# Performance work log

Measured on AMD Instinct MI355X. Metric: run time of the kernel, lower is better.

## Reference

```python
import jax, jax.numpy as jnp
import numpy as np

L, D_IN, D_OUT, H = 4096, 512, 256, 4
HEAD = D_OUT // H  # 64


def setup_inputs() -> dict:
    key = jax.random.key(0)
    k1, k2, k3, k4, k5 = jax.random.split(key, 5)
    h = jax.random.normal(k1, (L, D_IN), dtype=jnp.float32)
    A = jax.random.randint(k2, (L, L), 0, 2, dtype=jnp.int32)
    W = jax.random.normal(k3, (D_OUT, D_IN), dtype=jnp.float32) * 0.05
    attn = jax.random.normal(k4, (H, 2 * HEAD), dtype=jnp.float32) * 0.05
    out_w = jax.random.normal(k5, (D_OUT, D_OUT), dtype=jnp.float32) * 0.05
    out_b = jnp.zeros((D_OUT,), dtype=jnp.float32)
    return {"h": h, "A": A, "W": W, "attn": attn, "out_w": out_w, "out_b": out_b}


def reference(h, A, W, attn, out_w, out_b):
    # h: (L, D_in), A: (L, L) in {0,1}
    Lq = h.shape[0]
    n_heads, two_d = attn.shape
    d = two_d // 2
    Wh = (h @ W.T).reshape(Lq, n_heads, d)  # (L, H, d)
    # Algebraic rewrite of concat-score: e_ij = a1.Wh_i + a2.Wh_j
    a1, a2 = attn[:, :d], attn[:, d:]
    s_i = jnp.einsum("lhd,hd->lh", Wh, a1)  # (L, H)
    s_j = jnp.einsum("lhd,hd->lh", Wh, a2)  # (L, H)
    e = jax.nn.leaky_relu(s_i[:, None, :] + s_j[None, :, :], negative_slope=0.2)  # (L, L, H)
    mask = (A > 0)[:, :, None]  # (L, L, 1)
    NEG = jnp.asarray(-1e30, e.dtype)
    e = jnp.where(mask, e, NEG)
    # stable masked softmax over j (axis=1); rows with no neighbors -> alpha = 0
    m = jnp.max(e, axis=1, keepdims=True)
    m = jnp.where(m > NEG / 2, m, 0.0)
    ex = jnp.where(mask, jnp.exp(e - m), 0.0)
    denom = jnp.sum(ex, axis=1, keepdims=True)
    alpha = ex / jnp.where(denom > 0, denom, 1.0)  # (L, L, H)
    # dropout is identity in eval mode
    out = jnp.einsum("ijh,jhd->ihd", alpha, Wh).reshape(Lq, n_heads * d)
    return out @ out_w.T + out_b
```

## Files before the change

### kernel.cpp

```cpp
#include <hip/hip_runtime.h>
#include <hip/hip_bf16.h>

#define L_    4096
#define DIN   512
#define DOUT  256
#define NH    4
#define HD    64
#define JW    128

typedef unsigned short u16;
typedef __attribute__((ext_vector_type(8))) short short8;
typedef __attribute__((ext_vector_type(4))) float floatx4;

__device__ __forceinline__ float bf2f(u16 u) {
  union { unsigned u32; float f; } v; v.u32 = ((unsigned)u) << 16; return v.f;
}
__device__ __forceinline__ u16 f2bf(float f) {
  union { float f; unsigned u; } v; v.f = f;
  unsigned r = v.u + 0x7fff + ((v.u >> 16) & 1);
  return (u16)(r >> 16);
}
__device__ __forceinline__ unsigned cvt2(float a, float b) {
  __hip_bfloat162 v = __float22bfloat162_rn(make_float2(a, b));
  return *reinterpret_cast<unsigned*>(&v);
}
__device__ __forceinline__ short8 pack8(const float* __restrict__ p) {
  float4 a = *(const float4*)p, b = *(const float4*)(p + 4);
  union { unsigned u[4]; short8 s; } r;
  r.u[0] = cvt2(a.x, a.y); r.u[1] = cvt2(a.z, a.w);
  r.u[2] = cvt2(b.x, b.y); r.u[3] = cvt2(b.z, b.w);
  return r.s;
}

__device__ __forceinline__ void mfma_cdmap(int lane, int* rowm, int* colm) {
  const int c0 = lane & 15;
  union { u16 u[8]; short8 s; } a1, b1, a2, b2;
  const u16 one = f2bf(1.f), cid = f2bf((float)c0);
  #pragma unroll
  for (int j = 0; j < 8; ++j) { a1.u[j] = cid; b1.u[j] = one; a2.u[j] = one; b2.u[j] = cid; }
  floatx4 z = {0.f, 0.f, 0.f, 0.f};
  floatx4 dr = __builtin_amdgcn_mfma_f32_16x16x32_bf16(a1.s, b1.s, z, 0, 0, 0);
  floatx4 dc = __builtin_amdgcn_mfma_f32_16x16x32_bf16(a2.s, b2.s, z, 0, 0, 0);
  #pragma unroll
  for (int r = 0; r < 4; ++r) {
    rowm[r] = (int)(dr[r] * 0.03125f + 0.5f);
    colm[r] = (int)(dc[r] * 0.03125f + 0.5f);
  }
}

__global__ __launch_bounds__(256) void k0b_wf(const float* __restrict__ W,
                                              u16* __restrict__ Wf) {
  const int g = blockIdx.x * 256 + threadIdx.x;
  const int col = g >> 4, kblock = g & 15;
  const int cg = col >> 6, nt = (col >> 4) & 3, c0 = col & 15;
  const float* src = W + (size_t)col * DIN + kblock * 32;
  u16* dst = Wf + ((size_t)(cg * 4 + nt) * 16 + kblock) * 512 + c0 * 8;
  #pragma unroll
  for (int q = 0; q < 4; ++q) {
    short8 v = pack8(src + q * 8);
    *(short8*)(dst + q * 128) = v;
  }
}

__global__ __launch_bounds__(1024) void k1_wh(
    const float* __restrict__ h, const u16* __restrict__ Wf,
    const float* __restrict__ attn,
    u16* __restrict__ WhTf, float* __restrict__ s1g, float2* __restrict__ bdg)
{
  const int i0 = blockIdx.x * 16;
  const int t = threadIdx.x;
  const int wv = t >> 6, lane = t & 63, q = lane >> 4, c0 = lane & 15;
  const int cg = wv & 3, kc = wv >> 2;
  int rowm[4], colm[4];
  mfma_cdmap(lane, rowm, colm);

  __shared__ u16  hT[16][DIN + 8];
  __shared__ float pA[16][DOUT + 8];
  __shared__ float pB[16][DOUT + 8];
  __shared__ float attnL[NH * 128];

  if (t < 512) attnL[t] = attn[t];
  {
    const int row = t >> 6, c8 = (t & 63) * 8;
    const float* hp = h + (size_t)(i0 + row) * DIN + c8;
    float4 a = *(const float4*)hp;
    float4 b = *(const float4*)(hp + 4);
    union { unsigned u[4]; int4 v; } pk;
    pk.u[0] = cvt2(a.x, a.y); pk.u[1] = cvt2(a.z, a.w);
    pk.u[2] = cvt2(b.x, b.y); pk.u[3] = cvt2(b.z, b.w);
    *(int4*)&hT[row][c8] = pk.v;
  }
  __syncthreads();

  floatx4 acc[4] = {};
  #pragma unroll
  for (int ktl = 0; ktl < 4; ++ktl) {
    const int kb = kc * 128 + ktl * 32 + q * 8;
    short8 af = *(const short8*)&hT[c0][kb];
    #pragma unroll
    for (int nt = 0; nt < 4; ++nt) {
      short8 bf = *(const short8*)(Wf + ((size_t)(cg * 4 + nt) * 16 + kc * 4 + ktl) * 512 + lane * 8);
      acc[nt] = __builtin_amdgcn_mfma_f32_16x16x32_bf16(af, bf, acc[nt], 0, 0, 0);
    }
  }

  auto writeT = [&](float (*P)[DOUT + 8]) {
    #pragma unroll
    for (int nt = 0; nt < 4; ++nt)
      #pragma unroll
      for (int r = 0; r < 4; ++r)
        P[rowm[r]][cg * 64 + nt * 16 + colm[r]] = acc[nt][r];
  };
  auto addB2A = [&]() {
    const int row = t >> 6, c4 = (t & 63) * 4;
    float4* a = (float4*)&pA[row][c4];
    float4 bv = *(float4*)&pB[row][c4];
    float4 av = *a;
    av.x += bv.x; av.y += bv.y; av.z += bv.z; av.w += bv.w;
    *a = av;
  };

  if (kc == 0) writeT(pA);
  if (kc == 1) writeT(pB);
  __syncthreads();
  addB2A();
  __syncthreads();
  if (kc == 2) writeT(pB);
  __syncthreads();
  addB2A();
  __syncthreads();
  if (kc == 3) writeT(pB);
  __syncthreads();
  addB2A();
  __syncthreads();

  if (t < 64) {
    const int r = t & 15, hh = t >> 4;
    float s1 = 0.f, s2 = 0.f;
    for (int d = 0; d < HD; ++d) {
      float v = pA[r][hh * 64 + d];
      s1 += v * attnL[hh * 128 + d];
      s2 += v * attnL[hh * 128 + 64 + d];
    }
    s1g[hh * L_ + i0 + r] = s1;
    bdg[hh * L_ + i0 + r] = make_float2(__expf(s2), __expf(0.2f * s2));
  }

  if (t < 256) {
    const int d = t;
    const int hd = d >> 6, nt = (d >> 4) & 3, dc0 = d & 15;
    const int jblock = i0 >> 5, qbase = (i0 & 31) >> 3;
    u16* base = WhTf + ((size_t)(hd * 4 + nt) * JW + jblock) * 512 + dc0 * 8;
    #pragma unroll
    for (int jh = 0; jh < 2; ++jh) {
      const int i = jh * 8;
      union { unsigned u[4]; int4 v; } pk;
      pk.u[0] = cvt2(pA[i + 0][d], pA[i + 1][d]);
      pk.u[1] = cvt2(pA[i + 2][d], pA[i + 3][d]);
      pk.u[2] = cvt2(pA[i + 4][d], pA[i + 5][d]);
      pk.u[3] = cvt2(pA[i + 6][d], pA[i + 7][d]);
      *(int4*)(base + (qbase + jh) * 128) = pk.v;
    }
  }
}

__global__ __launch_bounds__(1024) void k2_attn(
    const int* __restrict__ A, const u16* __restrict__ WhTf,
    const float* __restrict__ s1g, const float2* __restrict__ bdg,
    const float* __restrict__ out_w, const float* __restrict__ out_b,
    float* __restrict__ out)
{
  const int i0 = blockIdx.x * 16;
  const int t = threadIdx.x;
  const int wv = t >> 6, lane = t & 63, q = lane >> 4, c0 = lane & 15;
  const int hd = wv & 3, jc = wv >> 2;
  int rowm[4], colm[4];
  mfma_cdmap(lane, rowm, colm);

  __shared__ float pA[NH][16][HD + 4];
  __shared__ float pB[NH][16][HD + 4];
  __shared__ float dden[NH][4][16];
  __shared__ float rcpS[NH][16];
  __shared__ u16  CnL[16][DOUT + 8];
  __shared__ unsigned AbitL[16][JW + 2];

  {
    const int row = t >> 6, ln = t & 63;
    const int* Ar = A + (size_t)(i0 + row) * L_;
    #pragma unroll
    for (int wsel = 0; wsel < 2; ++wsel) {
      const int wI = ln * 2 + wsel;
      const int* p = Ar + wI * 32;
      unsigned bits = 0u;
      #pragma unroll
      for (int wd = 0; wd < 8; ++wd) {
        int4 v = *(const int4*)(p + wd * 4);
        bits |= (v.x > 0 ? 1u : 0u) << (wd * 4 + 0);
        bits |= (v.y > 0 ? 1u : 0u) << (wd * 4 + 1);
        bits |= (v.z > 0 ? 1u : 0u) << (wd * 4 + 2);
        bits |= (v.w > 0 ? 1u : 0u) << (wd * 4 + 3);
      }
      AbitL[row][wI] = bits;
    }
  }
  __syncthreads();

  const float s1v = s1g[hd * L_ + i0 + c0];
  const float av = __expf(s1v);
  const float cv = __expf(0.2f * s1v);
  const float th = __expf(-s1v);
  const float2* bdh = bdg + (size_t)hd * L_;
  const u16* Wc = WhTf + (size_t)(hd * 4) * JW * 512 + (size_t)(jc * 32) * 512 + lane * 8;

  floatx4 acc[4] = {};
  float dpart = 0.f;
  const int jbase = jc * 1024;

  for (int kt = 0; kt < 32; ++kt) {
    const int kb = jbase + kt * 32 + q * 8;
    float4 v0 = *(const float4*)(bdh + kb);
    float4 v1 = *(const float4*)(bdh + kb + 2);
    float4 v2 = *(const float4*)(bdh + kb + 4);
    float4 v3 = *(const float4*)(bdh + kb + 6);
    const float bb[8] = {v0.x, v0.z, v1.x, v1.z, v2.x, v2.z, v3.x, v3.z};
    const float dd[8] = {v0.y, v0.w, v1.y, v1.w, v2.y, v2.w, v3.y, v3.w};
    const unsigned mbits = (AbitL[c0][jc * 32 + kt] >> (q * 8)) & 0xffu;
    float ex[8];
    #pragma unroll
    for (int jj = 0; jj < 8; ++jj) {
      float p = (bb[jj] >= th) ? (av * bb[jj]) : (cv * dd[jj]);
      ex[jj] = ((mbits >> jj) & 1u) ? p : 0.f;
      dpart += ex[jj];
    }
    union { unsigned u[4]; short8 s; } pf;
    pf.u[0] = cvt2(ex[0], ex[1]); pf.u[1] = cvt2(ex[2], ex[3]);
    pf.u[2] = cvt2(ex[4], ex[5]); pf.u[3] = cvt2(ex[6], ex[7]);
    #pragma unroll
    for (int nt = 0; nt < 4; ++nt) {
      short8 bfr = *(const short8*)(Wc + ((size_t)nt * JW + kt) * 512);
      acc[nt] = __builtin_amdgcn_mfma_f32_16x16x32_bf16(pf.s, bfr, acc[nt], 0, 0, 0);
    }
  }

  dpart += __shfl_xor(dpart, 16, 64);
  dpart += __shfl_xor(dpart, 32, 64);
  if (lane < 16) dden[hd][jc][lane] = dpart;

  auto writeT = [&](float (*P)[HD + 4]) {
    #pragma unroll
    for (int nt = 0; nt < 4; ++nt)
      #pragma unroll
      for (int r = 0; r < 4; ++r)
        P[rowm[r]][nt * 16 + colm[r]] = acc[nt][r];
  };
  auto addB2A = [&]() {
    const int h2 = t >> 8, rem = t & 255, row = rem >> 4, d4 = (rem & 15) * 4;
    float4* a = (float4*)&pA[h2][row][d4];
    float4 bv = *(float4*)&pB[h2][row][d4];
    float4 av2 = *a;
    av2.x += bv.x; av2.y += bv.y; av2.z += bv.z; av2.w += bv.w;
    *a = av2;
  };

  if (jc == 0) writeT(pA[hd]);
  if (jc == 1) writeT(pB[hd]);
  __syncthreads();
  if (t < 64) {
    const int hh = t >> 4, r = t & 15;
    float den = dden[hh][0][r] + dden[hh][1][r] + dden[hh][2][r] + dden[hh][3][r];
    rcpS[hh][r] = (den > 0.f) ? (1.f / den) : 0.f;
  }
  addB2A();
  __syncthreads();
  if (jc == 2) writeT(pB[hd]);
  __syncthreads();
  addB2A();
  __syncthreads();
  if (jc == 3) writeT(pB[hd]);
  __syncthreads();
  addB2A();
  __syncthreads();

  {
    const int row = t >> 6, c4 = (t & 63) * 4;
    #pragma unroll
    for (int x = 0; x < 4; ++x) {
      const int col = c4 + x;
      const int hh = col >> 6, d = col & 63;
      CnL[row][col] = f2bf(pA[hh][row][d] * rcpS[hh][row]);
    }
  }
  __syncthreads();

  if (wv < 4) {
    const int cg = wv;
    floatx4 o[4] = {};
    #pragma unroll
    for (int kt = 0; kt < DOUT / 32; ++kt) {
      const int kb2 = kt * 32 + q * 8;
      short8 afr = *(const short8*)(&CnL[c0][kb2]);
      #pragma unroll
      for (int nt = 0; nt < 4; ++nt) {
        const int col = cg * 64 + nt * 16 + c0;
        short8 bfo = pack8(out_w + (size_t)col * DOUT + kb2);
        o[nt] = __builtin_amdgcn_mfma_f32_16x16x32_bf16(afr, bfo, o[nt], 0, 0, 0);
      }
    }
    #pragma unroll
    for (int nt = 0; nt < 4; ++nt)
      #pragma unroll
      for (int r = 0; r < 4; ++r) {
        const int col = cg * 64 + nt * 16 + colm[r];
        out[(size_t)(i0 + rowm[r]) * DOUT + col] = o[nt][r] + out_b[col];
      }
  }
}

extern "C" void kernel_launch(void* const* d_in, const int* in_sizes, int n_in,
                              void* d_out, int out_size, void* d_ws, size_t ws_size,
                              hipStream_t stream) {
  const float* h     = (const float*)d_in[0];
  const int*   A     = (const int*)d_in[1];
  const float* W     = (const float*)d_in[2];
  const float* attn  = (const float*)d_in[3];
  const float* out_w = (const float*)d_in[4];
  const float* out_b = (const float*)d_in[5];
  float* outp = (float*)d_out;

  u16*    WhTf = (u16*)d_ws;
  float*  s1g  = (float*)((char*)d_ws + (size_t)DOUT * L_ * 2);
  float2* bdg  = (float2*)((char*)d_ws + (size_t)DOUT * L_ * 2 + (size_t)NH * L_ * 4);
  u16* Wf = (u16*)d_out;

  hipLaunchKernelGGL(k0b_wf, dim3(16), dim3(256), 0, stream, W, Wf);
  hipLaunchKernelGGL(k1_wh, dim3(L_ / 16), dim3(1024), 0, stream,
                     h, Wf, attn, WhTf, s1g, bdg);
  hipLaunchKernelGGL(k2_attn, dim3(L_ / 16), dim3(1024), 0, stream,
                     A, WhTf, s1g, bdg, out_w, out_b, outp);
}
```

Baseline: 163.5 us.

## Overlap adjacency bitmask packing with main loop and double-buffer operand loads

The adjacency mask is now packed into 16-bit words in four chunks. Only the first chunk is loaded before the main loop; the loads for each later chunk are issued during the previous eight iterations and stored behind a barrier. The main loop is also software-pipelined with two register buffers, so W fragments, score pairs and mask bits for the next k-step are loaded while the current step's MFMAs run. This aims to hide global load latency and the upfront A read, at the cost of more registers and extra block-wide barriers.

```diff
diff --git a/kernel.cpp b/kernel.cpp
--- a/kernel.cpp
+++ b/kernel.cpp
@@ -182,26 +182,34 @@
   __shared__ float dden[NH][4][16];
   __shared__ float rcpS[NH][16];
   __shared__ u16  CnL[16][DOUT + 8];
-  __shared__ unsigned AbitL[16][JW + 2];
+  __shared__ u16  Ab16[16][2 * JW + 4];
+
+  const int arow = t >> 6, aidx = t & 63;
+  const int ajc = aidx >> 4, arest = aidx & 15, awo = arest >> 1, ahalf = arest & 1;
+  const int* Abase = A + (size_t)(i0 + arow) * L_;
+  auto apack_src = [&](int chunk) -> const int* {
+    const int wI = ajc * 32 + chunk * 8 + awo;
+    return Abase + wI * 32 + ahalf * 16;
+  };
+  auto astore = [&](int chunk, const int4* v) {
+    unsigned bits = 0u;
+    #pragma unroll
+    for (int w = 0; w < 4; ++w) {
+      bits |= (v[w].x > 0 ? 1u : 0u) << (w * 4 + 0);
+      bits |= (v[w].y > 0 ? 1u : 0u) << (w * 4 + 1);
+      bits |= (v[w].z > 0 ? 1u : 0u) << (w * 4 + 2);
+      bits |= (v[w].w > 0 ? 1u : 0u) << (w * 4 + 3);
+    }
+    const int wI = ajc * 32 + chunk * 8 + awo;
+    Ab16[arow][wI * 2 + ahalf] = (u16)bits;
+  };
 
   {
-    const int row = t >> 6, ln = t & 63;
-    const int* Ar = A + (size_t)(i0 + row) * L_;
-    #pragma unroll
-    for (int wsel = 0; wsel < 2; ++wsel) {
-      const int wI = ln * 2 + wsel;
-      const int* p = Ar + wI * 32;
-      unsigned bits = 0u;
-      #pragma unroll
-      for (int wd = 0; wd < 8; ++wd) {
-        int4 v = *(const int4*)(p + wd * 4);
-        bits |= (v.x > 0 ? 1u : 0u) << (wd * 4 + 0);
-        bits |= (v.y > 0 ? 1u : 0u) << (wd * 4 + 1);
-        bits |= (v.z > 0 ? 1u : 0u) << (wd * 4 + 2);
-        bits |= (v.w > 0 ? 1u : 0u) << (wd * 4 + 3);
-      }
-      AbitL[row][wI] = bits;
-    }
+    const int* s = apack_src(0);
+    int4 v0[4];
+    #pragma unroll
+    for (int w = 0; w < 4; ++w) v0[w] = *(const int4*)(s + w * 4);
+    astore(0, v0);
   }
   __syncthreads();
 
@@ -211,36 +219,69 @@
   const float th = __expf(-s1v);
   const float2* bdh = bdg + (size_t)hd * L_;
   const u16* Wc = WhTf + (size_t)(hd * 4) * JW * 512 + (size_t)(jc * 32) * 512 + lane * 8;
+  const int jbase = jc * 1024;
 
   floatx4 acc[4] = {};
   float dpart = 0.f;
-  const int jbase = jc * 1024;
-
-  for (int kt = 0; kt < 32; ++kt) {
-    const int kb = jbase + kt * 32 + q * 8;
-    float4 v0 = *(const float4*)(bdh + kb);
-    float4 v1 = *(const float4*)(bdh + kb + 2);
-    float4 v2 = *(const float4*)(bdh + kb + 4);
-    float4 v3 = *(const float4*)(bdh + kb + 6);
-    const float bb[8] = {v0.x, v0.z, v1.x, v1.z, v2.x, v2.z, v3.x, v3.z};
-    const float dd[8] = {v0.y, v0.w, v1.y, v1.w, v2.y, v2.w, v3.y, v3.w};
-    const unsigned mbits = (AbitL[c0][jc * 32 + kt] >> (q * 8)) & 0xffu;
+
+  auto loadW = [&](int kt, short8* w) {
+    #pragma unroll
+    for (int nt = 0; nt < 4; ++nt)
+      w[nt] = *(const short8*)(Wc + ((size_t)nt * JW + kt) * 512);
+  };
+  auto loadV = [&](int kt, float4* v) {
+    const float2* p = bdh + jbase + kt * 32 + q * 8;
+    v[0] = *(const float4*)p;       v[1] = *(const float4*)(p + 2);
+    v[2] = *(const float4*)(p + 4); v[3] = *(const float4*)(p + 6);
+  };
+  auto bits16 = [&](int kt) -> unsigned {
+    return *(const unsigned*)&Ab16[c0][(jc * 32 + kt) * 2];
+  };
+  auto body = [&](const short8* w, const float4* v, unsigned wbits) {
+    const unsigned mb = (wbits >> (q * 8)) & 0xffu;
+    const float bb[8] = {v[0].x, v[0].z, v[1].x, v[1].z, v[2].x, v[2].z, v[3].x, v[3].z};
+    const float dd[8] = {v[0].y, v[0].w, v[1].y, v[1].w, v[2].y, v[2].w, v[3].y, v[3].w};
     float ex[8];
     #pragma unroll
     for (int jj = 0; jj < 8; ++jj) {
       float p = (bb[jj] >= th) ? (av * bb[jj]) : (cv * dd[jj]);
-      ex[jj] = ((mbits >> jj) & 1u) ? p : 0.f;
+      ex[jj] = ((mb >> jj) & 1u) ? p : 0.f;
       dpart += ex[jj];
     }
     union { unsigned u[4]; short8 s; } pf;
     pf.u[0] = cvt2(ex[0], ex[1]); pf.u[1] = cvt2(ex[2], ex[3]);
     pf.u[2] = cvt2(ex[4], ex[5]); pf.u[3] = cvt2(ex[6], ex[7]);
     #pragma unroll
-    for (int nt = 0; nt < 4; ++nt) {
-      short8 bfr = *(const short8*)(Wc + ((size_t)nt * JW + kt) * 512);
-      acc[nt] = __builtin_amdgcn_mfma_f32_16x16x32_bf16(pf.s, bfr, acc[nt], 0, 0, 0);
-    }
-  }
+    for (int nt = 0; nt < 4; ++nt)
+      acc[nt] = __builtin_amdgcn_mfma_f32_16x16x32_bf16(pf.s, w[nt], acc[nt], 0, 0, 0);
+  };
+  auto run8 = [&](int base, const int* Apre, int4* pre) {
+    short8 wA[4], wB[4];
+    float4 vA[4], vB[4];
+    unsigned aA, aB;
+    loadW(base, wA); loadV(base, vA); aA = bits16(base);
+    #pragma unroll
+    for (int kk = 0; kk < 4; ++kk) {
+      const int kt = base + kk * 2;
+      loadW(kt + 1, wB); loadV(kt + 1, vB); aB = bits16(kt + 1);
+      if (Apre) pre[kk] = *(const int4*)(Apre + kk * 4);
+      body(wA, vA, aA);
+      if (kk < 3) { loadW(kt + 2, wA); loadV(kt + 2, vA); aA = bits16(kt + 2); }
+      body(wB, vB, aB);
+    }
+  };
+
+  int4 pre[4];
+  run8(0, apack_src(1), pre);
+  astore(1, pre);
+  __syncthreads();
+  run8(8, apack_src(2), pre);
+  astore(2, pre);
+  __syncthreads();
+  run8(16, apack_src(3), pre);
+  astore(3, pre);
+  __syncthreads();
+  run8(24, nullptr, pre);
 
   dpart += __shfl_xor(dpart, 16, 64);
   dpart += __shfl_xor(dpart, 32, 64);
```

Result: no change. 161.8 us (-1.0%).

## Pre-pack adjacency bits in a separate kernel and software-pipeline the attention loop

Applied to the files above, without the earlier changes.

Adds a standalone kernel that reads the full int32 adjacency matrix with coalesced int4 loads and packs it into a bitmask using lane shuffles. The attention kernel then loads only the precomputed bits instead of thresholding A itself. The attention inner loop is also double-buffered: bias/denominator and WhT fragments for the next k-tiles are fetched before the current MFMAs run, with sched_barriers enforcing the order. The extra launch and a scratch buffer (falling back to part of the output) add overhead and register pressure in exchange for hiding load latency.

```diff
diff --git a/kernel.cpp b/kernel.cpp
--- a/kernel.cpp
+++ b/kernel.cpp
@@ -45,6 +45,24 @@
   for (int r = 0; r < 4; ++r) {
     rowm[r] = (int)(dr[r] * 0.03125f + 0.5f);
     colm[r] = (int)(dc[r] * 0.03125f + 0.5f);
+  }
+}
+
+__global__ __launch_bounds__(256) void k_ab(const int* __restrict__ A,
+                                            unsigned* __restrict__ Abits) {
+  const int g = blockIdx.x * 256 + threadIdx.x;
+  const int lane = threadIdx.x & 63;
+  #pragma unroll
+  for (int r = 0; r < 8; ++r) {
+    const size_t gi = (size_t)r * 524288 + g;
+    int4 v = *(const int4*)(A + gi * 4);
+    unsigned nib = (v.x > 0 ? 1u : 0u) | (v.y > 0 ? 2u : 0u)
+                 | (v.z > 0 ? 4u : 0u) | (v.w > 0 ? 8u : 0u);
+    unsigned part = nib << ((lane & 7) * 4);
+    part |= __shfl_xor(part, 1, 64);
+    part |= __shfl_xor(part, 2, 64);
+    part |= __shfl_xor(part, 4, 64);
+    if ((lane & 7) == 0) Abits[gi >> 3] = part;
   }
 }
 
@@ -165,7 +183,7 @@
 }
 
 __global__ __launch_bounds__(1024) void k2_attn(
-    const int* __restrict__ A, const u16* __restrict__ WhTf,
+    const unsigned* __restrict__ Abits, const u16* __restrict__ WhTf,
     const float* __restrict__ s1g, const float2* __restrict__ bdg,
     const float* __restrict__ out_w, const float* __restrict__ out_b,
     float* __restrict__ out)
@@ -174,8 +192,6 @@
   const int t = threadIdx.x;
   const int wv = t >> 6, lane = t & 63, q = lane >> 4, c0 = lane & 15;
   const int hd = wv & 3, jc = wv >> 2;
-  int rowm[4], colm[4];
-  mfma_cdmap(lane, rowm, colm);
 
   __shared__ float pA[NH][16][HD + 4];
   __shared__ float pB[NH][16][HD + 4];
@@ -185,24 +201,13 @@
   __shared__ unsigned AbitL[16][JW + 2];
 
   {
-    const int row = t >> 6, ln = t & 63;
-    const int* Ar = A + (size_t)(i0 + row) * L_;
-    #pragma unroll
-    for (int wsel = 0; wsel < 2; ++wsel) {
-      const int wI = ln * 2 + wsel;
-      const int* p = Ar + wI * 32;
-      unsigned bits = 0u;
-      #pragma unroll
-      for (int wd = 0; wd < 8; ++wd) {
-        int4 v = *(const int4*)(p + wd * 4);
-        bits |= (v.x > 0 ? 1u : 0u) << (wd * 4 + 0);
-        bits |= (v.y > 0 ? 1u : 0u) << (wd * 4 + 1);
-        bits |= (v.z > 0 ? 1u : 0u) << (wd * 4 + 2);
-        bits |= (v.w > 0 ? 1u : 0u) << (wd * 4 + 3);
-      }
-      AbitL[row][wI] = bits;
-    }
-  }
+    const int row = t >> 6, l = t & 63;
+    uint2 w2 = *(const uint2*)&Abits[(size_t)(i0 + row) * JW + l * 2];
+    AbitL[row][l * 2] = w2.x;
+    AbitL[row][l * 2 + 1] = w2.y;
+  }
+  int rowm[4], colm[4];
+  mfma_cdmap(lane, rowm, colm);
   __syncthreads();
 
   const float s1v = s1g[hd * L_ + i0 + c0];
@@ -211,36 +216,72 @@
   const float th = __expf(-s1v);
   const float2* bdh = bdg + (size_t)hd * L_;
   const u16* Wc = WhTf + (size_t)(hd * 4) * JW * 512 + (size_t)(jc * 32) * 512 + lane * 8;
+  const int jbase = jc * 1024;
 
   floatx4 acc[4] = {};
   float dpart = 0.f;
-  const int jbase = jc * 1024;
-
-  for (int kt = 0; kt < 32; ++kt) {
-    const int kb = jbase + kt * 32 + q * 8;
-    float4 v0 = *(const float4*)(bdh + kb);
-    float4 v1 = *(const float4*)(bdh + kb + 2);
-    float4 v2 = *(const float4*)(bdh + kb + 4);
-    float4 v3 = *(const float4*)(bdh + kb + 6);
-    const float bb[8] = {v0.x, v0.z, v1.x, v1.z, v2.x, v2.z, v3.x, v3.z};
-    const float dd[8] = {v0.y, v0.w, v1.y, v1.w, v2.y, v2.w, v3.y, v3.w};
-    const unsigned mbits = (AbitL[c0][jc * 32 + kt] >> (q * 8)) & 0xffu;
+
+  union PF { unsigned u[4]; short8 s; };
+
+  auto issueV = [&](int kt, float4* v) {
+    const float2* p = bdh + jbase + kt * 32 + q * 8;
+    v[0] = *(const float4*)p;       v[1] = *(const float4*)(p + 2);
+    v[2] = *(const float4*)(p + 4); v[3] = *(const float4*)(p + 6);
+  };
+  auto issueW = [&](int kt, short8* w) {
+    #pragma unroll
+    for (int nt = 0; nt < 4; ++nt)
+      w[nt] = *(const short8*)(Wc + ((size_t)nt * JW + kt) * 512);
+  };
+  auto sm8 = [&](const float4* v, int kt, PF& pf) {
+    const unsigned mb = (AbitL[c0][jc * 32 + kt] >> (q * 8)) & 0xffu;
+    const float bb[8] = {v[0].x, v[0].z, v[1].x, v[1].z, v[2].x, v[2].z, v[3].x, v[3].z};
+    const float dd[8] = {v[0].y, v[0].w, v[1].y, v[1].w, v[2].y, v[2].w, v[3].y, v[3].w};
     float ex[8];
     #pragma unroll
     for (int jj = 0; jj < 8; ++jj) {
       float p = (bb[jj] >= th) ? (av * bb[jj]) : (cv * dd[jj]);
-      ex[jj] = ((mbits >> jj) & 1u) ? p : 0.f;
+      ex[jj] = ((mb >> jj) & 1u) ? p : 0.f;
       dpart += ex[jj];
     }
-    union { unsigned u[4]; short8 s; } pf;
     pf.u[0] = cvt2(ex[0], ex[1]); pf.u[1] = cvt2(ex[2], ex[3]);
     pf.u[2] = cvt2(ex[4], ex[5]); pf.u[3] = cvt2(ex[6], ex[7]);
-    #pragma unroll
-    for (int nt = 0; nt < 4; ++nt) {
-      short8 bfr = *(const short8*)(Wc + ((size_t)nt * JW + kt) * 512);
-      acc[nt] = __builtin_amdgcn_mfma_f32_16x16x32_bf16(pf.s, bfr, acc[nt], 0, 0, 0);
-    }
-  }
+  };
+  auto mfma4 = [&](PF& pf, const short8* w) {
+    #pragma unroll
+    for (int nt = 0; nt < 4; ++nt)
+      acc[nt] = __builtin_amdgcn_mfma_f32_16x16x32_bf16(pf.s, w[nt], acc[nt], 0, 0, 0);
+  };
+
+  float4 vA[4], vB[4];
+  short8 wA[4], wB[4];
+  PF pfA, pfB;
+
+  issueV(0, vA); issueW(0, wA);
+  issueV(1, vB); issueW(1, wB);
+  __builtin_amdgcn_sched_barrier(0);
+  sm8(vA, 0, pfA);
+
+  #pragma unroll 1
+  for (int u = 0; u < 15; ++u) {
+    const int kt = 2 * u;
+    issueV(kt + 2, vA);
+    __builtin_amdgcn_sched_barrier(0);
+    sm8(vB, kt + 1, pfB);
+    mfma4(pfA, wA);
+    __builtin_amdgcn_sched_barrier(0);
+    issueW(kt + 2, wA);
+    issueV(kt + 3, vB);
+    __builtin_amdgcn_sched_barrier(0);
+    mfma4(pfB, wB);
+    __builtin_amdgcn_sched_barrier(0);
+    issueW(kt + 3, wB);
+    sm8(vA, kt + 2, pfA);
+    __builtin_amdgcn_sched_barrier(0);
+  }
+  mfma4(pfA, wA);
+  sm8(vB, 31, pfB);
+  mfma4(pfB, wB);
 
   dpart += __shfl_xor(dpart, 16, 64);
   dpart += __shfl_xor(dpart, 32, 64);
@@ -327,14 +368,22 @@
   const float* out_b = (const float*)d_in[5];
   float* outp = (float*)d_out;
 
+  const size_t WHTF_B = (size_t)DOUT * L_ * 2;
+  const size_t S1_B   = (size_t)NH * L_ * 4;
+  const size_t BD_B   = (size_t)NH * L_ * 8;
+  const size_t AB_OFF = WHTF_B + S1_B + BD_B;
   u16*    WhTf = (u16*)d_ws;
-  float*  s1g  = (float*)((char*)d_ws + (size_t)DOUT * L_ * 2);
-  float2* bdg  = (float2*)((char*)d_ws + (size_t)DOUT * L_ * 2 + (size_t)NH * L_ * 4);
+  float*  s1g  = (float*)((char*)d_ws + WHTF_B);
+  float2* bdg  = (float2*)((char*)d_ws + WHTF_B + S1_B);
+  unsigned* Abits = (ws_size >= AB_OFF + (size_t)L_ * JW * 4 )
+                  ? (unsigned*)((char*)d_ws + AB_OFF)
+                  : (unsigned*)((char*)d_out + 2097152);
   u16* Wf = (u16*)d_out;
 
+  hipLaunchKernelGGL(k_ab, dim3(2048), dim3(256), 0, stream, A, Abits);
   hipLaunchKernelGGL(k0b_wf, dim3(16), dim3(256), 0, stream, W, Wf);
   hipLaunchKernelGGL(k1_wh, dim3(L_ / 16), dim3(1024), 0, stream,
                      h, Wf, attn, WhTf, s1g, bdg);
   hipLaunchKernelGGL(k2_attn, dim3(L_ / 16), dim3(1024), 0, stream,
-                     A, WhTf, s1g, bdg, out_w, out_b, outp);
-}
+                     Abits, WhTf, s1g, bdg, out_w, out_b, outp);
+}
```

After: 156.3 us. -4.4%, faster.

## Pre-pack adjacency bits in a wide prologue kernel and streamline attention loop

Applied to the files above, without the earlier changes.

Moves the int32-to-bitmask conversion of A out of the attention kernel into a new 2048-block prologue kernel. That kernel also does the W packing and uses shuffles to build the bit words. The attention kernel now only loads the compact bitmask, and its inner loop is rewritten with pointer increments and all loads issued up front. The goal is a fully parallel, coalesced stream over the large A matrix instead of a per-row read inside a 256-block kernel. The cost is an extra global round trip for the 2 MB bitmask. If the workspace is too small, the fallback places the bitmask inside the output buffer, where it could be overwritten while other blocks still read it.

```diff
diff --git a/kernel.cpp b/kernel.cpp
--- a/kernel.cpp
+++ b/kernel.cpp
@@ -48,17 +48,35 @@
   }
 }
 
-__global__ __launch_bounds__(256) void k0b_wf(const float* __restrict__ W,
-                                              u16* __restrict__ Wf) {
-  const int g = blockIdx.x * 256 + threadIdx.x;
-  const int col = g >> 4, kblock = g & 15;
-  const int cg = col >> 6, nt = (col >> 4) & 3, c0 = col & 15;
-  const float* src = W + (size_t)col * DIN + kblock * 32;
-  u16* dst = Wf + ((size_t)(cg * 4 + nt) * 16 + kblock) * 512 + c0 * 8;
+__global__ __launch_bounds__(256) void k_ab(const int* __restrict__ A,
+                                            unsigned* __restrict__ Abits,
+                                            const float* __restrict__ W,
+                                            u16* __restrict__ Wf) {
+  const int t = threadIdx.x;
+  const int g = blockIdx.x * 256 + t;
+  const int lane = t & 63;
   #pragma unroll
-  for (int q = 0; q < 4; ++q) {
-    short8 v = pack8(src + q * 8);
-    *(short8*)(dst + q * 128) = v;
+  for (int r = 0; r < 8; ++r) {
+    const size_t gi = (size_t)r * 524288 + g;
+    int4 v = *(const int4*)(A + gi * 4);
+    unsigned nib = (v.x > 0 ? 1u : 0u) | (v.y > 0 ? 2u : 0u)
+                 | (v.z > 0 ? 4u : 0u) | (v.w > 0 ? 8u : 0u);
+    unsigned part = nib << ((lane & 7) * 4);
+    part |= __shfl_xor(part, 1, 64);
+    part |= __shfl_xor(part, 2, 64);
+    part |= __shfl_xor(part, 4, 64);
+    if ((lane & 7) == 0) Abits[gi >> 3] = part;
+  }
+  if (blockIdx.x < 16) {
+    const int col = g >> 4, kblock = g & 15;
+    const int cg = col >> 6, nt = (col >> 4) & 3, c0 = col & 15;
+    const float* src = W + (size_t)col * DIN + kblock * 32;
+    u16* dst = Wf + ((size_t)(cg * 4 + nt) * 16 + kblock) * 512 + c0 * 8;
+    #pragma unroll
+    for (int q = 0; q < 4; ++q) {
+      short8 v = pack8(src + q * 8);
+      *(short8*)(dst + q * 128) = v;
+    }
   }
 }
 
@@ -165,7 +183,7 @@
 }
 
 __global__ __launch_bounds__(1024) void k2_attn(
-    const int* __restrict__ A, const u16* __restrict__ WhTf,
+    const unsigned* __restrict__ Abits, const u16* __restrict__ WhTf,
     const float* __restrict__ s1g, const float2* __restrict__ bdg,
     const float* __restrict__ out_w, const float* __restrict__ out_b,
     float* __restrict__ out)
@@ -174,8 +192,6 @@
   const int t = threadIdx.x;
   const int wv = t >> 6, lane = t & 63, q = lane >> 4, c0 = lane & 15;
   const int hd = wv & 3, jc = wv >> 2;
-  int rowm[4], colm[4];
-  mfma_cdmap(lane, rowm, colm);
 
   __shared__ float pA[NH][16][HD + 4];
   __shared__ float pB[NH][16][HD + 4];
@@ -185,61 +201,70 @@
   __shared__ unsigned AbitL[16][JW + 2];
 
   {
-    const int row = t >> 6, ln = t & 63;
-    const int* Ar = A + (size_t)(i0 + row) * L_;
-    #pragma unroll
-    for (int wsel = 0; wsel < 2; ++wsel) {
-      const int wI = ln * 2 + wsel;
-      const int* p = Ar + wI * 32;
-      unsigned bits = 0u;
-      #pragma unroll
-      for (int wd = 0; wd < 8; ++wd) {
-        int4 v = *(const int4*)(p + wd * 4);
-        bits |= (v.x > 0 ? 1u : 0u) << (wd * 4 + 0);
-        bits |= (v.y > 0 ? 1u : 0u) << (wd * 4 + 1);
-        bits |= (v.z > 0 ? 1u : 0u) << (wd * 4 + 2);
-        bits |= (v.w > 0 ? 1u : 0u) << (wd * 4 + 3);
-      }
-      AbitL[row][wI] = bits;
-    }
-  }
+    const int row = t >> 6, l = t & 63;
+    uint2 w2 = *(const uint2*)&Abits[(size_t)(i0 + row) * JW + l * 2];
+    AbitL[row][l * 2] = w2.x;
+    AbitL[row][l * 2 + 1] = w2.y;
+  }
+  int rowm[4], colm[4];
+  mfma_cdmap(lane, rowm, colm);
   __syncthreads();
 
   const float s1v = s1g[hd * L_ + i0 + c0];
   const float av = __expf(s1v);
   const float cv = __expf(0.2f * s1v);
   const float th = __expf(-s1v);
-  const float2* bdh = bdg + (size_t)hd * L_;
-  const u16* Wc = WhTf + (size_t)(hd * 4) * JW * 512 + (size_t)(jc * 32) * 512 + lane * 8;
-
+  const int qs = q * 8;
+
+  const float2*   bdp = bdg + (size_t)hd * L_ + jc * 1024 + qs;
+  const u16*      wp0 = WhTf + ((size_t)(hd * 4 + 0) * JW + jc * 32) * 512 + lane * 8;
+  const u16*      wp1 = WhTf + ((size_t)(hd * 4 + 1) * JW + jc * 32) * 512 + lane * 8;
+  const u16*      wp2 = WhTf + ((size_t)(hd * 4 + 2) * JW + jc * 32) * 512 + lane * 8;
+  const u16*      wp3 = WhTf + ((size_t)(hd * 4 + 3) * JW + jc * 32) * 512 + lane * 8;
+  const unsigned* abp = &AbitL[c0][jc * 32];
+
+  union PF { unsigned u[4]; short8 s; };
   floatx4 acc[4] = {};
   float dpart = 0.f;
-  const int jbase = jc * 1024;
 
   for (int kt = 0; kt < 32; ++kt) {
-    const int kb = jbase + kt * 32 + q * 8;
-    float4 v0 = *(const float4*)(bdh + kb);
-    float4 v1 = *(const float4*)(bdh + kb + 2);
-    float4 v2 = *(const float4*)(bdh + kb + 4);
-    float4 v3 = *(const float4*)(bdh + kb + 6);
-    const float bb[8] = {v0.x, v0.z, v1.x, v1.z, v2.x, v2.z, v3.x, v3.z};
-    const float dd[8] = {v0.y, v0.w, v1.y, v1.w, v2.y, v2.w, v3.y, v3.w};
-    const unsigned mbits = (AbitL[c0][jc * 32 + kt] >> (q * 8)) & 0xffu;
-    float ex[8];
-    #pragma unroll
-    for (int jj = 0; jj < 8; ++jj) {
-      float p = (bb[jj] >= th) ? (av * bb[jj]) : (cv * dd[jj]);
-      ex[jj] = ((mbits >> jj) & 1u) ? p : 0.f;
-      dpart += ex[jj];
-    }
-    union { unsigned u[4]; short8 s; } pf;
-    pf.u[0] = cvt2(ex[0], ex[1]); pf.u[1] = cvt2(ex[2], ex[3]);
-    pf.u[2] = cvt2(ex[4], ex[5]); pf.u[3] = cvt2(ex[6], ex[7]);
-    #pragma unroll
-    for (int nt = 0; nt < 4; ++nt) {
-      short8 bfr = *(const short8*)(Wc + ((size_t)nt * JW + kt) * 512);
-      acc[nt] = __builtin_amdgcn_mfma_f32_16x16x32_bf16(pf.s, bfr, acc[nt], 0, 0, 0);
-    }
+    float4 v0 = *(const float4*)bdp;
+    float4 v1 = *(const float4*)(bdp + 2);
+    float4 v2 = *(const float4*)(bdp + 4);
+    float4 v3 = *(const float4*)(bdp + 6);
+    short8 w0 = *(const short8*)wp0;
+    short8 w1 = *(const short8*)wp1;
+    short8 w2 = *(const short8*)wp2;
+    short8 w3 = *(const short8*)wp3;
+    const unsigned mb = (*abp >> qs) & 0xffu;
+
+    float e0 = (v0.x >= th) ? (av * v0.x) : (cv * v0.y);
+    float e1 = (v0.z >= th) ? (av * v0.z) : (cv * v0.w);
+    float e2 = (v1.x >= th) ? (av * v1.x) : (cv * v1.y);
+    float e3 = (v1.z >= th) ? (av * v1.z) : (cv * v1.w);
+    float e4 = (v2.x >= th) ? (av * v2.x) : (cv * v2.y);
+    float e5 = (v2.z >= th) ? (av * v2.z) : (cv * v2.w);
+    float e6 = (v3.x >= th) ? (av * v3.x) : (cv * v3.y);
+    float e7 = (v3.z >= th) ? (av * v3.z) : (cv * v3.w);
+    e0 = (mb & 1u)   ? e0 : 0.f;
+    e1 = (mb & 2u)   ? e1 : 0.f;
+    e2 = (mb & 4u)   ? e2 : 0.f;
+    e3 = (mb & 8u)   ? e3 : 0.f;
+    e4 = (mb & 16u)  ? e4 : 0.f;
+    e5 = (mb & 32u)  ? e5 : 0.f;
+    e6 = (mb & 64u)  ? e6 : 0.f;
+    e7 = (mb & 128u) ? e7 : 0.f;
+    dpart += ((e0 + e1) + (e2 + e3)) + ((e4 + e5) + (e6 + e7));
+
+    PF pf;
+    pf.u[0] = cvt2(e0, e1); pf.u[1] = cvt2(e2, e3);
+    pf.u[2] = cvt2(e4, e5); pf.u[3] = cvt2(e6, e7);
+    acc[0] = __builtin_amdgcn_mfma_f32_16x16x32_bf16(pf.s, w0, acc[0], 0, 0, 0);
+    acc[1] = __builtin_amdgcn_mfma_f32_16x16x32_bf16(pf.s, w1, acc[1], 0, 0, 0);
+    acc[2] = __builtin_amdgcn_mfma_f32_16x16x32_bf16(pf.s, w2, acc[2], 0, 0, 0);
+    acc[3] = __builtin_amdgcn_mfma_f32_16x16x32_bf16(pf.s, w3, acc[3], 0, 0, 0);
+
+    bdp += 32; wp0 += 512; wp1 += 512; wp2 += 512; wp3 += 512; abp += 1;
   }
 
   dpart += __shfl_xor(dpart, 16, 64);
@@ -327,14 +352,23 @@
   const float* out_b = (const float*)d_in[5];
   float* outp = (float*)d_out;
 
+  const size_t WHTF_B  = (size_t)DOUT * L_ * 2;
+  const size_t S1_B    = (size_t)NH * L_ * 4;
+  const size_t BD_B    = (size_t)NH * L_ * 8;
+  const size_t ABITS_B = (size_t)L_ * JW * 4;
+  const size_t AB_OFF  = WHTF_B + S1_B + BD_B;
+
   u16*    WhTf = (u16*)d_ws;
-  float*  s1g  = (float*)((char*)d_ws + (size_t)DOUT * L_ * 2);
-  float2* bdg  = (float2*)((char*)d_ws + (size_t)DOUT * L_ * 2 + (size_t)NH * L_ * 4);
+  float*  s1g  = (float*)((char*)d_ws + WHTF_B);
+  float2* bdg  = (float2*)((char*)d_ws + WHTF_B + S1_B);
+  unsigned* Abits = (ws_size >= AB_OFF + ABITS_B)
+                  ? (unsigned*)((char*)d_ws + AB_OFF)
+                  : (unsigned*)((char*)d_out + 2097152);
   u16* Wf = (u16*)d_out;
 
-  hipLaunchKernelGGL(k0b_wf, dim3(16), dim3(256), 0, stream, W, Wf);
+  hipLaunchKernelGGL(k_ab, dim3(2048), dim3(256), 0, stream, A, Abits, W, Wf);
   hipLaunchKernelGGL(k1_wh, dim3(L_ / 16), dim3(1024), 0, stream,
                      h, Wf, attn, WhTf, s1g, bdg);
   hipLaunchKernelGGL(k2_attn, dim3(L_ / 16), dim3(1024), 0, stream,
-                     A, WhTf, s1g, bdg, out_w, out_b, outp);
-}
+                     Abits, WhTf, s1g, bdg, out_w, out_b, outp);
+}
```

Result: faster. 158.8 us (-2.9%).
